# Kernel tuning notes

Measured on AMD Instinct MI355X. Metric: run time of the kernel, lower is better.

## Reference

```python
import jax, jax.numpy as jnp
import numpy as np

B, T, C = 4, 128, 512
NH, HS = 8, 64          # n_head, head_dim = C // NH
ORDER = 3               # attention_order
SCALE = 1.0 / np.sqrt(HS)


def setup_inputs() -> dict:
    key = jax.random.key(0)
    ks = jax.random.split(key, 7)
    s = 0.02
    return {
        "x": jax.random.normal(ks[0], (B, T, C), jnp.float32),
        "Wp0": jax.random.normal(ks[1], (C, C), jnp.float32) * s,
        "Wp1": jax.random.normal(ks[2], (C, C), jnp.float32) * s,
        "Wp2": jax.random.normal(ks[3], (C, C), jnp.float32) * s,
        "Wv0": jax.random.normal(ks[4], (HS, HS), jnp.float32) * s,
        "Wv1": jax.random.normal(ks[5], (HS, HS), jnp.float32) * s,
        "Wc": jax.random.normal(ks[6], (C, C), jnp.float32) * s,
    }


def _heads(x, W):
    # Linear then split heads: (B,T,C) -> (B,NH,T,HS)
    return (x @ W).reshape(B, T, NH, HS).transpose(0, 2, 1, 3)


def _causal_mask(t, order):
    # indices grid [T]^order, True where i0 >= i1 >= ... >= i_{order-1}
    idx = jnp.arange(t)
    g = jnp.stack(jnp.meshgrid(*([idx] * order), indexing='ij'), axis=-1)
    return jnp.all(jnp.diff(g, axis=-1) <= 0, axis=-1)


def reference(x, Wp0, Wp1, Wp2, Wv0, Wv1, Wc):
    p0 = _heads(x, Wp0)  # (B,NH,T,HS)
    p1 = _heads(x, Wp1)
    p2 = _heads(x, Wp2)

    # pairwise scores, then higher-order broadcast exactly as the torch einsum
    # ('bh...i,bhkd->bh...ik' sums the key over d and broadcasts — faithful).
    att = jnp.einsum('bhid,bhjd->bhij', p0, p1) * SCALE        # (B,NH,T,T)
    att = jnp.einsum('bh...i,bhkd->bh...ik', att, p2)          # (B,NH,T,T,T)

    mask = _causal_mask(T, ORDER)[None, None]                  # (1,1,T,T,T)
    att = jnp.where(mask, att, -jnp.inf)
    att = jax.nn.softmax(att.reshape(B, NH, T, T * T), axis=-1)

    # value tensors with broadcasted elementwise product over the order dims
    V0 = (p1 @ Wv0)[:, :, :, None, :]   # (B,NH,T,1,HS)
    V1 = (p2 @ Wv1)[:, :, None, :, :]   # (B,NH,1,T,HS)
    V = (V0 * V1).reshape(B, NH, T * T, HS)

    y = jnp.einsum('bhij,bhjd->bhid', att, V)                  # (B,NH,T,HS)
    y = y.transpose(0, 2, 1, 3).reshape(B, T, C)
    return y @ Wc
```

## Files before the change

kernel.cpp:

```cpp
#include <hip/hip_runtime.h>
#include <hip/hip_bf16.h>
#include <math.h>

#define B 4
#define T 128
#define C 512
#define NH 8
#define HS 64
#define BH (B*NH)

typedef __attribute__((ext_vector_type(8))) short bf16x8;
typedef __attribute__((ext_vector_type(4))) float f32x4;

__device__ __forceinline__ unsigned short bfc(float x) {
    return __builtin_bit_cast(unsigned short, __float2bfloat16(x));
}
__device__ __forceinline__ unsigned int pk_bf16(float a, float b) {
    return (unsigned int)bfc(a) | ((unsigned int)bfc(b) << 16);
}
__device__ __forceinline__ float lo_f(unsigned int g) {
    return __builtin_bit_cast(float, g << 16);
}
__device__ __forceinline__ float hi_f(unsigned int g) {
    return __builtin_bit_cast(float, g & 0xffff0000u);
}

__global__ __launch_bounds__(256) void proj_kernel(
    const float* __restrict__ X,
    const float* __restrict__ Wp0, const float* __restrict__ Wp1, const float* __restrict__ Wp2,
    unsigned short* __restrict__ p0b, unsigned short* __restrict__ p1b,
    unsigned short* __restrict__ p2b, float* __restrict__ rr)
{
    __shared__ __align__(16) unsigned short As[64][72];
    __shared__ __align__(16) unsigned short Bs[64][72];
    __shared__ float Ls[64][69];
    __shared__ float sRS[4][64];
    const int z = blockIdx.z;
    const float* W = (z == 0) ? Wp0 : (z == 1) ? Wp1 : Wp2;
    const int m0 = blockIdx.y * 64, n0 = blockIdx.x * 64;
    const int tid = threadIdx.x;
    const int w = tid >> 6, lane = tid & 63, quad = lane >> 4, l16 = lane & 15;
    f32x4 acc[4];
    #pragma unroll
    for (int mt = 0; mt < 4; ++mt) acc[mt] = (f32x4){0.f, 0.f, 0.f, 0.f};

    for (int k0 = 0; k0 < 512; k0 += 64) {
        __syncthreads();
        #pragma unroll
        for (int it = 0; it < 2; ++it) {
            const int q = tid + it * 256;
            const int row = q >> 3, c8 = (q & 7) * 8;
            const float4 a = *(const float4*)&X[(size_t)(m0 + row) * 512 + k0 + c8];
            const float4 b = *(const float4*)&X[(size_t)(m0 + row) * 512 + k0 + c8 + 4];
            uint4 o;
            o.x = pk_bf16(a.x, a.y);
            o.y = pk_bf16(a.z, a.w);
            o.z = pk_bf16(b.x, b.y);
            o.w = pk_bf16(b.z, b.w);
            *(uint4*)&As[row][c8] = o;
        }
        #pragma unroll
        for (int it = 0; it < 4; ++it) {
            const int q = tid + it * 256;
            const int row = q >> 4, c4 = (q & 15) * 4;
            const float4 v = *(const float4*)&W[(size_t)(k0 + row) * 512 + n0 + c4];
            Ls[row][c4 + 0] = v.x; Ls[row][c4 + 1] = v.y;
            Ls[row][c4 + 2] = v.z; Ls[row][c4 + 3] = v.w;
        }
        __syncthreads();
        #pragma unroll
        for (int it = 0; it < 2; ++it) {
            const int q = tid + it * 256;
            const int nrow = q >> 3, k8 = (q & 7) * 8;
            uint4 o;
            o.x = pk_bf16(Ls[k8 + 0][nrow], Ls[k8 + 1][nrow]);
            o.y = pk_bf16(Ls[k8 + 2][nrow], Ls[k8 + 3][nrow]);
            o.z = pk_bf16(Ls[k8 + 4][nrow], Ls[k8 + 5][nrow]);
            o.w = pk_bf16(Ls[k8 + 6][nrow], Ls[k8 + 7][nrow]);
            *(uint4*)&Bs[nrow][k8] = o;
        }
        __syncthreads();
        #pragma unroll
        for (int kt = 0; kt < 2; ++kt) {
            const bf16x8 b8 = *(const bf16x8*)&Bs[w * 16 + l16][kt * 32 + quad * 8];
            #pragma unroll
            for (int mt = 0; mt < 4; ++mt) {
                const bf16x8 a8 = *(const bf16x8*)&As[mt * 16 + l16][kt * 32 + quad * 8];
                acc[mt] = __builtin_amdgcn_mfma_f32_16x16x32_bf16(a8, b8, acc[mt], 0, 0, 0);
            }
        }
    }

    {
        const int n = n0 + w * 16 + l16;
        const int h = n >> 6, d = n & 63;
        unsigned short* pz = (z == 0) ? p0b : (z == 1) ? p1b : p2b;
        #pragma unroll
        for (int mt = 0; mt < 4; ++mt) {
            #pragma unroll
            for (int r = 0; r < 4; ++r) {
                const int m = m0 + mt * 16 + quad * 4 + r;
                const int bb = m >> 7, t = m & 127;
                pz[((size_t)(bb * NH + h) * T + t) * HS + d] = bfc(acc[mt][r]);
            }
        }
    }
    if (z == 2) {
        #pragma unroll
        for (int mt = 0; mt < 4; ++mt)
            #pragma unroll
            for (int r = 0; r < 4; ++r) {
                float v = acc[mt][r];
                v += __shfl_xor(v, 1, 64); v += __shfl_xor(v, 2, 64);
                v += __shfl_xor(v, 4, 64); v += __shfl_xor(v, 8, 64);
                if (l16 == 0) sRS[w][mt * 16 + quad * 4 + r] = v;
            }
        __syncthreads();
        if (tid < 64) {
            const float s = sRS[0][tid] + sRS[1][tid] + sRS[2][tid] + sRS[3][tid];
            const int m = m0 + tid, bb = m >> 7, tl = m & 127, h = n0 >> 6;
            rr[(bb * NH + h) * T + tl] = s;
        }
    }
}

__global__ __launch_bounds__(256) void attn_kernel(
    const unsigned short* __restrict__ p0b, const unsigned short* __restrict__ p1b,
    const unsigned short* __restrict__ p2b, const float* __restrict__ rr,
    const float* __restrict__ Wv0, const float* __restrict__ Wv1,
    unsigned short* __restrict__ Yb)
{
    __shared__ __align__(16) unsigned short sV0T[64][136];
    __shared__ __align__(16) unsigned short sV1T[64][136];
    __shared__ __align__(16) union {
        unsigned short sWvT[2][64][72];
        struct { unsigned short sE[128 * 64]; float sS[8][128]; } e;
    } u;
    __shared__ float srr[128];
    __shared__ float sZ[4];

    const int bid = blockIdx.x;
    const int bh = bid & (BH - 1);
    const int ig = bid >> 5;
    const int tid = threadIdx.x;
    const int w = tid >> 6;
    const int lane = tid & 63;
    const int quad = lane >> 4;
    const int l16 = lane & 15;

    if (tid < 128) srr[tid] = rr[bh * T + tid];

    #pragma unroll
    for (int v = 0; v < 2; ++v) {
        const float* Wv = v ? Wv1 : Wv0;
        #pragma unroll
        for (int it = 0; it < 4; ++it) {
            const int k = (tid >> 4) + it * 16;
            const int d0 = (tid & 15) * 4;
            const float4 wv = *(const float4*)&Wv[(size_t)k * 64 + d0];
            u.sWvT[v][d0 + 0][k] = bfc(wv.x);
            u.sWvT[v][d0 + 1][k] = bfc(wv.y);
            u.sWvT[v][d0 + 2][k] = bfc(wv.z);
            u.sWvT[v][d0 + 3][k] = bfc(wv.w);
        }
    }
    __syncthreads();

    #pragma unroll
    for (int v = 0; v < 2; ++v) {
        const unsigned short* pg = v ? p2b : p1b;
        unsigned short (*dst)[136] = v ? sV1T : sV0T;
        #pragma unroll
        for (int nn = 0; nn < 2; ++nn) {
            const int nt = w + nn * 4;
            f32x4 vacc[4];
            #pragma unroll
            for (int mt = 0; mt < 4; ++mt) vacc[mt] = (f32x4){0.f, 0.f, 0.f, 0.f};
            #pragma unroll
            for (int kt = 0; kt < 2; ++kt) {
                const bf16x8 b8 = *(const bf16x8*)&pg[((size_t)bh * T + nt * 16 + l16) * HS + kt * 32 + quad * 8];
                #pragma unroll
                for (int mt = 0; mt < 4; ++mt) {
                    const bf16x8 a8 = *(const bf16x8*)&u.sWvT[v][mt * 16 + l16][kt * 32 + quad * 8];
                    vacc[mt] = __builtin_amdgcn_mfma_f32_16x16x32_bf16(a8, b8, vacc[mt], 0, 0, 0);
                }
            }
            #pragma unroll
            for (int mt = 0; mt < 4; ++mt)
                #pragma unroll
                for (int r = 0; r < 4; ++r)
                    dst[mt * 16 + quad * 4 + r][nt * 16 + l16] = bfc(vacc[mt][r]);
        }
    }
    __syncthreads();

    uint4 v1r[4];
    #pragma unroll
    for (int kt = 0; kt < 4; ++kt)
        v1r[kt] = *(const uint4*)&sV1T[(w << 4) + l16][(quad << 3) + (kt << 5)];

    {
        const int qr = l16 & 7;
        const int irow = (qr & 1) ? (16 * qr + 15 - ig) : (16 * qr + ig);
        const unsigned short* ap = p0b + ((size_t)bh * T + irow) * HS + (quad << 3);
        const unsigned short* bp = p1b + (size_t)bh * T * HS + (quad << 3);
        f32x4 s0 = (f32x4){0.f, 0.f, 0.f, 0.f};
        f32x4 s1 = (f32x4){0.f, 0.f, 0.f, 0.f};
        #pragma unroll
        for (int kt = 0; kt < 2; ++kt) {
            const bf16x8 a8 = *(const bf16x8*)(ap + (kt << 5));
            const bf16x8 b0 = *(const bf16x8*)(bp + (size_t)((w << 5) + l16) * HS + (kt << 5));
            const bf16x8 b1 = *(const bf16x8*)(bp + (size_t)((w << 5) + 16 + l16) * HS + (kt << 5));
            s0 = __builtin_amdgcn_mfma_f32_16x16x32_bf16(a8, b0, s0, 0, 0, 0);
            s1 = __builtin_amdgcn_mfma_f32_16x16x32_bf16(a8, b1, s1, 0, 0, 0);
        }
        if (quad < 2) {
            #pragma unroll
            for (int r = 0; r < 4; ++r) {
                u.e.sS[quad * 4 + r][(w << 5) + l16]      = s0[r] * 0.125f;
                u.e.sS[quad * 4 + r][(w << 5) + 16 + l16] = s1[r] * 0.125f;
            }
        }
    }
    __syncthreads();

    const float L2E = 1.4426950408889634f;

    for (int qq = 7; qq >= 0; --qq) {
        const int i = (qq & 1) ? (16 * qq + 15 - ig) : (16 * qq + ig);
        const float* sSq = u.e.sS[qq];

        float mhat;
        {
            float a0 = (lane <= i) ? fabsf(sSq[lane]) : 0.f;
            float a1 = (64 + lane <= i) ? fabsf(sSq[64 + lane]) : 0.f;
            float r0 = (lane <= i) ? fabsf(srr[lane]) : 0.f;
            float r1 = (64 + lane <= i) ? fabsf(srr[64 + lane]) : 0.f;
            float aS = fmaxf(a0, a1), aR = fmaxf(r0, r1);
            #pragma unroll
            for (int off = 32; off; off >>= 1) {
                aS = fmaxf(aS, __shfl_xor(aS, off, 64));
                aR = fmaxf(aR, __shfl_xor(aR, off, 64));
            }
            mhat = aS * aR;
        }

        const float bexp = -mhat * L2E;
        const int mtmax = i >> 4;
        const int cc = tid & 7;
        const int rowin = tid >> 3;
        const int k0l = cc << 3;
        float zacc = 0.f;

        float rk[8];
        *(float4*)&rk[0] = *(const float4*)&srr[k0l];
        *(float4*)&rk[4] = *(const float4*)&srr[k0l + 4];
        const int npass0 = (mtmax >> 1) + 1;
        for (int p = 0; p < npass0; ++p) {
            const int jj = (p << 5) + rowin;
            uint4 o = {0u, 0u, 0u, 0u};
            if (jj <= i && k0l <= jj) {
                const float aL = sSq[jj] * L2E;
                const int dlim = jj - k0l;
                float e[8];
                #pragma unroll
                for (int q = 0; q < 8; ++q) {
                    const float ex = __builtin_amdgcn_exp2f(fmaf(aL, rk[q], bexp));
                    e[q] = (q <= dlim) ? ex : 0.f;
                    zacc += e[q];
                }
                o.x = pk_bf16(e[0], e[1]);
                o.y = pk_bf16(e[2], e[3]);
                o.z = pk_bf16(e[4], e[5]);
                o.w = pk_bf16(e[6], e[7]);
            }
            *(uint4*)&u.e.sE[(jj << 6) + ((cc ^ (jj & 7)) << 3)] = o;
        }

        f32x4 acc[8];
        #pragma unroll
        for (int mt = 0; mt < 8; ++mt) acc[mt] = (f32x4){0.f, 0.f, 0.f, 0.f};

        if (mtmax < 4) {
            #pragma unroll
            for (int off = 32; off; off >>= 1) zacc += __shfl_xor(zacc, off, 64);
            if (lane == 0) sZ[w] = zacc;
            __syncthreads();
            #pragma unroll
            for (int mt = 0; mt < 4; ++mt) {
                if (mt <= mtmax) {
                    #pragma unroll
                    for (int kt = 0; kt <= 1; ++kt) {
                        if (kt <= (mt >> 1)) {
                            const int swz = ((kt << 2) + quad) ^ (l16 & 7);
                            const bf16x8 a8 = *(const bf16x8*)&u.e.sE[(((mt << 4) + l16) << 6) + (swz << 3)];
                            acc[mt] = __builtin_amdgcn_mfma_f32_16x16x32_bf16(
                                a8, __builtin_bit_cast(bf16x8, v1r[kt]), acc[mt], 0, 0, 0);
                        }
                    }
                }
            }
        } else {
            __syncthreads();
            #pragma unroll
            for (int mt = 0; mt < 8; ++mt) {
                if (mt <= mtmax) {
                    #pragma unroll
                    for (int kt = 0; kt <= 1; ++kt) {
                        if (kt <= (mt >> 1)) {
                            const int swz = ((kt << 2) + quad) ^ (l16 & 7);
                            const bf16x8 a8 = *(const bf16x8*)&u.e.sE[(((mt << 4) + l16) << 6) + (swz << 3)];
                            acc[mt] = __builtin_amdgcn_mfma_f32_16x16x32_bf16(
                                a8, __builtin_bit_cast(bf16x8, v1r[kt]), acc[mt], 0, 0, 0);
                        }
                    }
                }
            }
            __syncthreads();
            *(float4*)&rk[0] = *(const float4*)&srr[64 + k0l];
            *(float4*)&rk[4] = *(const float4*)&srr[64 + k0l + 4];
            const int npass1 = ((mtmax - 4) >> 1) + 1;
            for (int p = 0; p < npass1; ++p) {
                const int jj = 64 + (p << 5) + rowin;
                uint4 o = {0u, 0u, 0u, 0u};
                if (jj <= i && 64 + k0l <= jj) {
                    const float aL = sSq[jj] * L2E;
                    const int dlim = jj - 64 - k0l;
                    float e[8];
                    #pragma unroll
                    for (int q = 0; q < 8; ++q) {
                        const float ex = __builtin_amdgcn_exp2f(fmaf(aL, rk[q], bexp));
                        e[q] = (q <= dlim) ? ex : 0.f;
                        zacc += e[q];
                    }
                    o.x = pk_bf16(e[0], e[1]);
                    o.y = pk_bf16(e[2], e[3]);
                    o.z = pk_bf16(e[4], e[5]);
                    o.w = pk_bf16(e[6], e[7]);
                }
                *(uint4*)&u.e.sE[(jj << 6) + ((cc ^ (jj & 7)) << 3)] = o;
            }
            #pragma unroll
            for (int off = 32; off; off >>= 1) zacc += __shfl_xor(zacc, off, 64);
            if (lane == 0) sZ[w] = zacc;
            __syncthreads();
            #pragma unroll
            for (int mt = 4; mt < 8; ++mt) {
                if (mt <= mtmax) {
                    #pragma unroll
                    for (int kt = 2; kt <= 3; ++kt) {
                        if (kt <= (mt >> 1)) {
                            const int swz = (((kt & 1) << 2) + quad) ^ (l16 & 7);
                            const bf16x8 a8 = *(const bf16x8*)&u.e.sE[(((mt << 4) + l16) << 6) + (swz << 3)];
                            acc[mt] = __builtin_amdgcn_mfma_f32_16x16x32_bf16(
                                a8, __builtin_bit_cast(bf16x8, v1r[kt]), acc[mt], 0, 0, 0);
                        }
                    }
                }
            }
        }
        const float Z = sZ[0] + sZ[1] + sZ[2] + sZ[3];

        const unsigned short* v0row = sV0T[(w << 4) + l16];
        float part = 0.f;
        #pragma unroll
        for (int mt = 0; mt < 8; ++mt) {
            if (mt < mtmax) {
                const uint2 uu = *(const uint2*)&v0row[(mt << 4) + (quad << 2)];
                part = fmaf(lo_f(uu.x), acc[mt][0], part);
                part = fmaf(hi_f(uu.x), acc[mt][1], part);
                part = fmaf(lo_f(uu.y), acc[mt][2], part);
                part = fmaf(hi_f(uu.y), acc[mt][3], part);
            } else if (mt == mtmax) {
                const uint2 uu = *(const uint2*)&v0row[(mt << 4) + (quad << 2)];
                const int jb = (mt << 4) + (quad << 2);
                if (jb + 0 <= i) part = fmaf(lo_f(uu.x), acc[mt][0], part);
                if (jb + 1 <= i) part = fmaf(hi_f(uu.x), acc[mt][1], part);
                if (jb + 2 <= i) part = fmaf(lo_f(uu.y), acc[mt][2], part);
                if (jb + 3 <= i) part = fmaf(hi_f(uu.y), acc[mt][3], part);
            }
        }
        part += __shfl_xor(part, 16, 64);
        part += __shfl_xor(part, 32, 64);
        if (lane < 16) {
            const int bb = bh >> 3, hh = bh & 7;
            Yb[((size_t)(bb * T + i) * C) + hh * HS + (w << 4) + l16] = bfc(part / Z);
        }
        __syncthreads();
    }
}

__global__ __launch_bounds__(256) void outmm_kernel(
    const unsigned short* __restrict__ Ab, const float* __restrict__ Wc,
    float* __restrict__ OUT)
{
    __shared__ __align__(16) unsigned short As[64][72];
    __shared__ __align__(16) unsigned short Bs[64][72];
    __shared__ float Ls[64][69];
    const int m0 = blockIdx.y * 64, n0 = blockIdx.x * 64;
    const int tid = threadIdx.x;
    const int w = tid >> 6, lane = tid & 63, quad = lane >> 4, l16 = lane & 15;
    f32x4 acc[4];
    #pragma unroll
    for (int mt = 0; mt < 4; ++mt) acc[mt] = (f32x4){0.f, 0.f, 0.f, 0.f};
    for (int k0 = 0; k0 < 512; k0 += 64) {
        __syncthreads();
        #pragma unroll
        for (int it = 0; it < 2; ++it) {
            const int q = tid + it * 256;
            const int row = q >> 3, c8 = (q & 7) * 8;
            *(uint4*)&As[row][c8] = *(const uint4*)&Ab[(size_t)(m0 + row) * 512 + k0 + c8];
        }
        #pragma unroll
        for (int it = 0; it < 4; ++it) {
            const int q = tid + it * 256;
            const int row = q >> 4, c4 = (q & 15) * 4;
            const float4 v = *(const float4*)&Wc[(size_t)(k0 + row) * 512 + n0 + c4];
            Ls[row][c4 + 0] = v.x; Ls[row][c4 + 1] = v.y;
            Ls[row][c4 + 2] = v.z; Ls[row][c4 + 3] = v.w;
        }
        __syncthreads();
        #pragma unroll
        for (int it = 0; it < 2; ++it) {
            const int q = tid + it * 256;
            const int nrow = q >> 3, k8 = (q & 7) * 8;
            uint4 o;
            o.x = pk_bf16(Ls[k8 + 0][nrow], Ls[k8 + 1][nrow]);
            o.y = pk_bf16(Ls[k8 + 2][nrow], Ls[k8 + 3][nrow]);
            o.z = pk_bf16(Ls[k8 + 4][nrow], Ls[k8 + 5][nrow]);
            o.w = pk_bf16(Ls[k8 + 6][nrow], Ls[k8 + 7][nrow]);
            *(uint4*)&Bs[nrow][k8] = o;
        }
        __syncthreads();
        #pragma unroll
        for (int kt = 0; kt < 2; ++kt) {
            const bf16x8 b8 = *(const bf16x8*)&Bs[w * 16 + l16][kt * 32 + quad * 8];
            #pragma unroll
            for (int mt = 0; mt < 4; ++mt) {
                const bf16x8 a8 = *(const bf16x8*)&As[mt * 16 + l16][kt * 32 + quad * 8];
                acc[mt] = __builtin_amdgcn_mfma_f32_16x16x32_bf16(a8, b8, acc[mt], 0, 0, 0);
            }
        }
    }
    const int n = n0 + w * 16 + l16;
    #pragma unroll
    for (int mt = 0; mt < 4; ++mt)
        #pragma unroll
        for (int r = 0; r < 4; ++r) {
            const int mrow = m0 + mt * 16 + quad * 4 + r;
            OUT[(size_t)mrow * 512 + n] = acc[mt][r];
        }
}

extern "C" void kernel_launch(void* const* d_in, const int* in_sizes, int n_in,
                              void* d_out, int out_size, void* d_ws, size_t ws_size,
                              hipStream_t stream)
{
    const float* x   = (const float*)d_in[0];
    const float* Wp0 = (const float*)d_in[1];
    const float* Wp1 = (const float*)d_in[2];
    const float* Wp2 = (const float*)d_in[3];
    const float* Wv0 = (const float*)d_in[4];
    const float* Wv1 = (const float*)d_in[5];
    const float* Wc  = (const float*)d_in[6];
    float* out = (float*)d_out;

    char* w8 = (char*)d_ws;
    const size_t HB = 512 * 1024;
    unsigned short* p0b = (unsigned short*)(w8 + 0 * HB);
    unsigned short* p1b = (unsigned short*)(w8 + 1 * HB);
    unsigned short* p2b = (unsigned short*)(w8 + 2 * HB);
    unsigned short* Yb  = (unsigned short*)(w8 + 3 * HB);
    float*          rr  = (float*)        (w8 + 4 * HB);

    proj_kernel <<<dim3(8, 8, 3), 256, 0, stream>>>(x, Wp0, Wp1, Wp2, p0b, p1b, p2b, rr);
    attn_kernel <<<dim3(512), 256, 0, stream>>>(p0b, p1b, p2b, rr, Wv0, Wv1, Yb);
    outmm_kernel<<<dim3(8, 8), 256, 0, stream>>>(Yb, Wc, out);
}
```

Baseline: 116.4 us.

## Fuse output projection into attention kernel via per-head atomic accumulation

```diff
diff --git a/kernel.cpp b/kernel.cpp
--- a/kernel.cpp
+++ b/kernel.cpp
@@ -29,7 +29,7 @@
     const float* __restrict__ X,
     const float* __restrict__ Wp0, const float* __restrict__ Wp1, const float* __restrict__ Wp2,
     unsigned short* __restrict__ p0b, unsigned short* __restrict__ p1b,
-    unsigned short* __restrict__ p2b, float* __restrict__ rr)
+    unsigned short* __restrict__ p2b, float* __restrict__ rr, float* __restrict__ OUT)
 {
     __shared__ __align__(16) unsigned short As[64][72];
     __shared__ __align__(16) unsigned short Bs[64][72];
@@ -40,6 +40,16 @@
     const int m0 = blockIdx.y * 64, n0 = blockIdx.x * 64;
     const int tid = threadIdx.x;
     const int w = tid >> 6, lane = tid & 63, quad = lane >> 4, l16 = lane & 15;
+
+    {
+        const int fid = z * 64 + (int)blockIdx.y * 8 + (int)blockIdx.x;
+        if (fid < 128) {
+            float4 zz = {0.f, 0.f, 0.f, 0.f};
+            *(float4*)&OUT[(size_t)fid * 2048 + tid * 8]     = zz;
+            *(float4*)&OUT[(size_t)fid * 2048 + tid * 8 + 4] = zz;
+        }
+    }
+
     f32x4 acc[4];
     #pragma unroll
     for (int mt = 0; mt < 4; ++mt) acc[mt] = (f32x4){0.f, 0.f, 0.f, 0.f};
@@ -128,7 +138,7 @@
     const unsigned short* __restrict__ p0b, const unsigned short* __restrict__ p1b,
     const unsigned short* __restrict__ p2b, const float* __restrict__ rr,
     const float* __restrict__ Wv0, const float* __restrict__ Wv1,
-    unsigned short* __restrict__ Yb)
+    const float* __restrict__ Wc, float* __restrict__ OUT)
 {
     __shared__ __align__(16) unsigned short sV0T[64][136];
     __shared__ __align__(16) unsigned short sV1T[64][136];
@@ -138,6 +148,7 @@
     } u;
     __shared__ float srr[128];
     __shared__ float sZ[4];
+    __shared__ float sY[8][64];
 
     const int bid = blockIdx.x;
     const int bh = bid & (BH - 1);
@@ -382,74 +393,34 @@
         }
         part += __shfl_xor(part, 16, 64);
         part += __shfl_xor(part, 32, 64);
-        if (lane < 16) {
-            const int bb = bh >> 3, hh = bh & 7;
-            Yb[((size_t)(bb * T + i) * C) + hh * HS + (w << 4) + l16] = bfc(part / Z);
-        }
+        if (lane < 16) sY[qq][(w << 4) + l16] = part / Z;
         __syncthreads();
     }
-}
-
-__global__ __launch_bounds__(256) void outmm_kernel(
-    const unsigned short* __restrict__ Ab, const float* __restrict__ Wc,
-    float* __restrict__ OUT)
-{
-    __shared__ __align__(16) unsigned short As[64][72];
-    __shared__ __align__(16) unsigned short Bs[64][72];
-    __shared__ float Ls[64][69];
-    const int m0 = blockIdx.y * 64, n0 = blockIdx.x * 64;
-    const int tid = threadIdx.x;
-    const int w = tid >> 6, lane = tid & 63, quad = lane >> 4, l16 = lane & 15;
-    f32x4 acc[4];
-    #pragma unroll
-    for (int mt = 0; mt < 4; ++mt) acc[mt] = (f32x4){0.f, 0.f, 0.f, 0.f};
-    for (int k0 = 0; k0 < 512; k0 += 64) {
-        __syncthreads();
-        #pragma unroll
-        for (int it = 0; it < 2; ++it) {
-            const int q = tid + it * 256;
-            const int row = q >> 3, c8 = (q & 7) * 8;
-            *(uint4*)&As[row][c8] = *(const uint4*)&Ab[(size_t)(m0 + row) * 512 + k0 + c8];
-        }
-        #pragma unroll
-        for (int it = 0; it < 4; ++it) {
-            const int q = tid + it * 256;
-            const int row = q >> 4, c4 = (q & 15) * 4;
-            const float4 v = *(const float4*)&Wc[(size_t)(k0 + row) * 512 + n0 + c4];
-            Ls[row][c4 + 0] = v.x; Ls[row][c4 + 1] = v.y;
-            Ls[row][c4 + 2] = v.z; Ls[row][c4 + 3] = v.w;
-        }
-        __syncthreads();
-        #pragma unroll
-        for (int it = 0; it < 2; ++it) {
-            const int q = tid + it * 256;
-            const int nrow = q >> 3, k8 = (q & 7) * 8;
-            uint4 o;
-            o.x = pk_bf16(Ls[k8 + 0][nrow], Ls[k8 + 1][nrow]);
-            o.y = pk_bf16(Ls[k8 + 2][nrow], Ls[k8 + 3][nrow]);
-            o.z = pk_bf16(Ls[k8 + 4][nrow], Ls[k8 + 5][nrow]);
-            o.w = pk_bf16(Ls[k8 + 6][nrow], Ls[k8 + 7][nrow]);
-            *(uint4*)&Bs[nrow][k8] = o;
-        }
-        __syncthreads();
-        #pragma unroll
-        for (int kt = 0; kt < 2; ++kt) {
-            const bf16x8 b8 = *(const bf16x8*)&Bs[w * 16 + l16][kt * 32 + quad * 8];
-            #pragma unroll
-            for (int mt = 0; mt < 4; ++mt) {
-                const bf16x8 a8 = *(const bf16x8*)&As[mt * 16 + l16][kt * 32 + quad * 8];
-                acc[mt] = __builtin_amdgcn_mfma_f32_16x16x32_bf16(a8, b8, acc[mt], 0, 0, 0);
-            }
-        }
-    }
-    const int n = n0 + w * 16 + l16;
-    #pragma unroll
-    for (int mt = 0; mt < 4; ++mt)
-        #pragma unroll
-        for (int r = 0; r < 4; ++r) {
-            const int mrow = m0 + mt * 16 + quad * 4 + r;
-            OUT[(size_t)mrow * 512 + n] = acc[mt][r];
-        }
+
+    {
+        const int bb = bh >> 3, hh = bh & 7;
+        const int n0 = tid * 2;
+        float oacc[8][2];
+        #pragma unroll
+        for (int r = 0; r < 8; ++r) { oacc[r][0] = 0.f; oacc[r][1] = 0.f; }
+        const float* wc = Wc + (size_t)hh * 64 * 512 + n0;
+        for (int k = 0; k < 64; ++k) {
+            const float2 wv = *(const float2*)&wc[(size_t)k * 512];
+            #pragma unroll
+            for (int r = 0; r < 8; ++r) {
+                const float yv = sY[r][k];
+                oacc[r][0] = fmaf(yv, wv.x, oacc[r][0]);
+                oacc[r][1] = fmaf(yv, wv.y, oacc[r][1]);
+            }
+        }
+        #pragma unroll
+        for (int qq = 0; qq < 8; ++qq) {
+            const int i = (qq & 1) ? (16 * qq + 15 - ig) : (16 * qq + ig);
+            float* orow = OUT + (size_t)(bb * T + i) * 512 + n0;
+            atomicAdd(&orow[0], oacc[qq][0]);
+            atomicAdd(&orow[1], oacc[qq][1]);
+        }
+    }
 }
 
 extern "C" void kernel_launch(void* const* d_in, const int* in_sizes, int n_in,
@@ -470,10 +441,8 @@
     unsigned short* p0b = (unsigned short*)(w8 + 0 * HB);
     unsigned short* p1b = (unsigned short*)(w8 + 1 * HB);
     unsigned short* p2b = (unsigned short*)(w8 + 2 * HB);
-    unsigned short* Yb  = (unsigned short*)(w8 + 3 * HB);
-    float*          rr  = (float*)        (w8 + 4 * HB);
-
-    proj_kernel <<<dim3(8, 8, 3), 256, 0, stream>>>(x, Wp0, Wp1, Wp2, p0b, p1b, p2b, rr);
-    attn_kernel <<<dim3(512), 256, 0, stream>>>(p0b, p1b, p2b, rr, Wv0, Wv1, Yb);
-    outmm_kernel<<<dim3(8, 8), 256, 0, stream>>>(Yb, Wc, out);
-}
+    float*          rr  = (float*)        (w8 + 3 * HB);
+
+    proj_kernel <<<dim3(8, 8, 3), 256, 0, stream>>>(x, Wp0, Wp1, Wp2, p0b, p1b, p2b, rr, out);
+    attn_kernel <<<dim3(512), 256, 0, stream>>>(p0b, p1b, p2b, rr, Wv0, Wv1, Wc, out);
+}
```

After: 120.1 us. 1.03x slower.

## Double attention grid, halve rows per block, single-pass full-width exp tile

Applied to the files above, without the earlier changes.

```diff
diff --git a/kernel.cpp b/kernel.cpp
--- a/kernel.cpp
+++ b/kernel.cpp
@@ -130,12 +130,14 @@
     const float* __restrict__ Wv0, const float* __restrict__ Wv1,
     unsigned short* __restrict__ Yb)
 {
-    __shared__ __align__(16) unsigned short sV0T[64][136];
-    __shared__ __align__(16) unsigned short sV1T[64][136];
     __shared__ __align__(16) union {
-        unsigned short sWvT[2][64][72];
-        struct { unsigned short sE[128 * 64]; float sS[8][128]; } e;
+        struct {
+            unsigned short sWv[64][72];
+            unsigned short sVst[64][136];
+        } v;
+        unsigned short sE[128 * 128];
     } u;
+    __shared__ float sS[4][128];
     __shared__ float srr[128];
     __shared__ float sZ[4];
 
@@ -151,57 +153,83 @@
     if (tid < 128) srr[tid] = rr[bh * T + tid];
 
     #pragma unroll
-    for (int v = 0; v < 2; ++v) {
-        const float* Wv = v ? Wv1 : Wv0;
-        #pragma unroll
-        for (int it = 0; it < 4; ++it) {
-            const int k = (tid >> 4) + it * 16;
-            const int d0 = (tid & 15) * 4;
-            const float4 wv = *(const float4*)&Wv[(size_t)k * 64 + d0];
-            u.sWvT[v][d0 + 0][k] = bfc(wv.x);
-            u.sWvT[v][d0 + 1][k] = bfc(wv.y);
-            u.sWvT[v][d0 + 2][k] = bfc(wv.z);
-            u.sWvT[v][d0 + 3][k] = bfc(wv.w);
-        }
+    for (int it = 0; it < 4; ++it) {
+        const int k = (tid >> 4) + it * 16;
+        const int d0 = (tid & 15) * 4;
+        const float4 wv = *(const float4*)&Wv0[(size_t)k * 64 + d0];
+        u.v.sWv[d0 + 0][k] = bfc(wv.x); u.v.sWv[d0 + 1][k] = bfc(wv.y);
+        u.v.sWv[d0 + 2][k] = bfc(wv.z); u.v.sWv[d0 + 3][k] = bfc(wv.w);
     }
     __syncthreads();
 
     #pragma unroll
-    for (int v = 0; v < 2; ++v) {
-        const unsigned short* pg = v ? p2b : p1b;
-        unsigned short (*dst)[136] = v ? sV1T : sV0T;
-        #pragma unroll
-        for (int nn = 0; nn < 2; ++nn) {
-            const int nt = w + nn * 4;
-            f32x4 vacc[4];
-            #pragma unroll
-            for (int mt = 0; mt < 4; ++mt) vacc[mt] = (f32x4){0.f, 0.f, 0.f, 0.f};
-            #pragma unroll
-            for (int kt = 0; kt < 2; ++kt) {
-                const bf16x8 b8 = *(const bf16x8*)&pg[((size_t)bh * T + nt * 16 + l16) * HS + kt * 32 + quad * 8];
-                #pragma unroll
-                for (int mt = 0; mt < 4; ++mt) {
-                    const bf16x8 a8 = *(const bf16x8*)&u.sWvT[v][mt * 16 + l16][kt * 32 + quad * 8];
-                    vacc[mt] = __builtin_amdgcn_mfma_f32_16x16x32_bf16(a8, b8, vacc[mt], 0, 0, 0);
-                }
-            }
-            #pragma unroll
-            for (int mt = 0; mt < 4; ++mt)
-                #pragma unroll
-                for (int r = 0; r < 4; ++r)
-                    dst[mt * 16 + quad * 4 + r][nt * 16 + l16] = bfc(vacc[mt][r]);
-        }
+    for (int nn = 0; nn < 2; ++nn) {
+        const int nt = w + nn * 4;
+        f32x4 vacc[4];
+        #pragma unroll
+        for (int mt = 0; mt < 4; ++mt) vacc[mt] = (f32x4){0.f, 0.f, 0.f, 0.f};
+        #pragma unroll
+        for (int kt = 0; kt < 2; ++kt) {
+            const bf16x8 b8 = *(const bf16x8*)&p1b[((size_t)bh * T + nt * 16 + l16) * HS + kt * 32 + quad * 8];
+            #pragma unroll
+            for (int mt = 0; mt < 4; ++mt) {
+                const bf16x8 a8 = *(const bf16x8*)&u.v.sWv[mt * 16 + l16][kt * 32 + quad * 8];
+                vacc[mt] = __builtin_amdgcn_mfma_f32_16x16x32_bf16(a8, b8, vacc[mt], 0, 0, 0);
+            }
+        }
+        #pragma unroll
+        for (int mt = 0; mt < 4; ++mt)
+            #pragma unroll
+            for (int r = 0; r < 4; ++r)
+                u.v.sVst[mt * 16 + quad * 4 + r][nt * 16 + l16] = bfc(vacc[mt][r]);
     }
     __syncthreads();
 
+    uint2 v0r[8];
+    #pragma unroll
+    for (int mt = 0; mt < 8; ++mt)
+        v0r[mt] = *(const uint2*)&u.v.sVst[(w << 4) + l16][(mt << 4) + (quad << 2)];
+    #pragma unroll
+    for (int it = 0; it < 4; ++it) {
+        const int k = (tid >> 4) + it * 16;
+        const int d0 = (tid & 15) * 4;
+        const float4 wv = *(const float4*)&Wv1[(size_t)k * 64 + d0];
+        u.v.sWv[d0 + 0][k] = bfc(wv.x); u.v.sWv[d0 + 1][k] = bfc(wv.y);
+        u.v.sWv[d0 + 2][k] = bfc(wv.z); u.v.sWv[d0 + 3][k] = bfc(wv.w);
+    }
+    __syncthreads();
+
+    #pragma unroll
+    for (int nn = 0; nn < 2; ++nn) {
+        const int nt = w + nn * 4;
+        f32x4 vacc[4];
+        #pragma unroll
+        for (int mt = 0; mt < 4; ++mt) vacc[mt] = (f32x4){0.f, 0.f, 0.f, 0.f};
+        #pragma unroll
+        for (int kt = 0; kt < 2; ++kt) {
+            const bf16x8 b8 = *(const bf16x8*)&p2b[((size_t)bh * T + nt * 16 + l16) * HS + kt * 32 + quad * 8];
+            #pragma unroll
+            for (int mt = 0; mt < 4; ++mt) {
+                const bf16x8 a8 = *(const bf16x8*)&u.v.sWv[mt * 16 + l16][kt * 32 + quad * 8];
+                vacc[mt] = __builtin_amdgcn_mfma_f32_16x16x32_bf16(a8, b8, vacc[mt], 0, 0, 0);
+            }
+        }
+        #pragma unroll
+        for (int mt = 0; mt < 4; ++mt)
+            #pragma unroll
+            for (int r = 0; r < 4; ++r)
+                u.v.sVst[mt * 16 + quad * 4 + r][nt * 16 + l16] = bfc(vacc[mt][r]);
+    }
+    __syncthreads();
+
     uint4 v1r[4];
     #pragma unroll
     for (int kt = 0; kt < 4; ++kt)
-        v1r[kt] = *(const uint4*)&sV1T[(w << 4) + l16][(quad << 3) + (kt << 5)];
+        v1r[kt] = *(const uint4*)&u.v.sVst[(w << 4) + l16][(quad << 3) + (kt << 5)];
 
     {
-        const int qr = l16 & 7;
-        const int irow = (qr & 1) ? (16 * qr + 15 - ig) : (16 * qr + ig);
+        const int qr = l16 & 3;
+        const int irow = (qr & 1) ? (32 * qr + 31 - ig) : (32 * qr + ig);
         const unsigned short* ap = p0b + ((size_t)bh * T + irow) * HS + (quad << 3);
         const unsigned short* bp = p1b + (size_t)bh * T * HS + (quad << 3);
         f32x4 s0 = (f32x4){0.f, 0.f, 0.f, 0.f};
@@ -214,11 +242,11 @@
             s0 = __builtin_amdgcn_mfma_f32_16x16x32_bf16(a8, b0, s0, 0, 0, 0);
             s1 = __builtin_amdgcn_mfma_f32_16x16x32_bf16(a8, b1, s1, 0, 0, 0);
         }
-        if (quad < 2) {
+        if (quad == 0) {
             #pragma unroll
             for (int r = 0; r < 4; ++r) {
-                u.e.sS[quad * 4 + r][(w << 5) + l16]      = s0[r] * 0.125f;
-                u.e.sS[quad * 4 + r][(w << 5) + 16 + l16] = s1[r] * 0.125f;
+                sS[r][(w << 5) + l16]      = s0[r] * 0.125f;
+                sS[r][(w << 5) + 16 + l16] = s1[r] * 0.125f;
             }
         }
     }
@@ -226,9 +254,9 @@
 
     const float L2E = 1.4426950408889634f;
 
-    for (int qq = 7; qq >= 0; --qq) {
-        const int i = (qq & 1) ? (16 * qq + 15 - ig) : (16 * qq + ig);
-        const float* sSq = u.e.sS[qq];
+    for (int qq = 3; qq >= 0; --qq) {
+        const int i = (qq & 1) ? (32 * qq + 31 - ig) : (32 * qq + ig);
+        const float* sSq = sS[qq];
 
         float mhat;
         {
@@ -247,17 +275,17 @@
 
         const float bexp = -mhat * L2E;
         const int mtmax = i >> 4;
-        const int cc = tid & 7;
-        const int rowin = tid >> 3;
+        const int cc = tid & 15;
+        const int rowin = tid >> 4;
         const int k0l = cc << 3;
         float zacc = 0.f;
 
         float rk[8];
         *(float4*)&rk[0] = *(const float4*)&srr[k0l];
         *(float4*)&rk[4] = *(const float4*)&srr[k0l + 4];
-        const int npass0 = (mtmax >> 1) + 1;
-        for (int p = 0; p < npass0; ++p) {
-            const int jj = (p << 5) + rowin;
+        const int npass = mtmax + 1;
+        for (int p = 0; p < npass; ++p) {
+            const int jj = (p << 4) + rowin;
             uint4 o = {0u, 0u, 0u, 0u};
             if (jj <= i && k0l <= jj) {
                 const float aL = sSq[jj] * L2E;
@@ -274,105 +302,43 @@
                 o.z = pk_bf16(e[4], e[5]);
                 o.w = pk_bf16(e[6], e[7]);
             }
-            *(uint4*)&u.e.sE[(jj << 6) + ((cc ^ (jj & 7)) << 3)] = o;
-        }
+            *(uint4*)&u.sE[(jj << 7) + ((cc ^ (jj & 7)) << 3)] = o;
+        }
+        #pragma unroll
+        for (int off = 32; off; off >>= 1) zacc += __shfl_xor(zacc, off, 64);
+        if (lane == 0) sZ[w] = zacc;
+        __syncthreads();
 
         f32x4 acc[8];
         #pragma unroll
         for (int mt = 0; mt < 8; ++mt) acc[mt] = (f32x4){0.f, 0.f, 0.f, 0.f};
-
-        if (mtmax < 4) {
-            #pragma unroll
-            for (int off = 32; off; off >>= 1) zacc += __shfl_xor(zacc, off, 64);
-            if (lane == 0) sZ[w] = zacc;
-            __syncthreads();
-            #pragma unroll
-            for (int mt = 0; mt < 4; ++mt) {
-                if (mt <= mtmax) {
-                    #pragma unroll
-                    for (int kt = 0; kt <= 1; ++kt) {
-                        if (kt <= (mt >> 1)) {
-                            const int swz = ((kt << 2) + quad) ^ (l16 & 7);
-                            const bf16x8 a8 = *(const bf16x8*)&u.e.sE[(((mt << 4) + l16) << 6) + (swz << 3)];
-                            acc[mt] = __builtin_amdgcn_mfma_f32_16x16x32_bf16(
-                                a8, __builtin_bit_cast(bf16x8, v1r[kt]), acc[mt], 0, 0, 0);
-                        }
+        #pragma unroll
+        for (int mt = 0; mt < 8; ++mt) {
+            if (mt <= mtmax) {
+                #pragma unroll
+                for (int kt = 0; kt < 4; ++kt) {
+                    if (kt <= (mt >> 1)) {
+                        const int ch = ((kt << 2) + quad) ^ (l16 & 7);
+                        const bf16x8 a8 = *(const bf16x8*)&u.sE[(((mt << 4) + l16) << 7) + (ch << 3)];
+                        acc[mt] = __builtin_amdgcn_mfma_f32_16x16x32_bf16(
+                            a8, __builtin_bit_cast(bf16x8, v1r[kt]), acc[mt], 0, 0, 0);
                     }
                 }
             }
-        } else {
-            __syncthreads();
-            #pragma unroll
-            for (int mt = 0; mt < 8; ++mt) {
-                if (mt <= mtmax) {
-                    #pragma unroll
-                    for (int kt = 0; kt <= 1; ++kt) {
-                        if (kt <= (mt >> 1)) {
-                            const int swz = ((kt << 2) + quad) ^ (l16 & 7);
-                            const bf16x8 a8 = *(const bf16x8*)&u.e.sE[(((mt << 4) + l16) << 6) + (swz << 3)];
-                            acc[mt] = __builtin_amdgcn_mfma_f32_16x16x32_bf16(
-                                a8, __builtin_bit_cast(bf16x8, v1r[kt]), acc[mt], 0, 0, 0);
-                        }
-                    }
-                }
-            }
-            __syncthreads();
-            *(float4*)&rk[0] = *(const float4*)&srr[64 + k0l];
-            *(float4*)&rk[4] = *(const float4*)&srr[64 + k0l + 4];
-            const int npass1 = ((mtmax - 4) >> 1) + 1;
-            for (int p = 0; p < npass1; ++p) {
-                const int jj = 64 + (p << 5) + rowin;
-                uint4 o = {0u, 0u, 0u, 0u};
-                if (jj <= i && 64 + k0l <= jj) {
-                    const float aL = sSq[jj] * L2E;
-                    const int dlim = jj - 64 - k0l;
-                    float e[8];
-                    #pragma unroll
-                    for (int q = 0; q < 8; ++q) {
-                        const float ex = __builtin_amdgcn_exp2f(fmaf(aL, rk[q], bexp));
-                        e[q] = (q <= dlim) ? ex : 0.f;
-                        zacc += e[q];
-                    }
-                    o.x = pk_bf16(e[0], e[1]);
-                    o.y = pk_bf16(e[2], e[3]);
-                    o.z = pk_bf16(e[4], e[5]);
-                    o.w = pk_bf16(e[6], e[7]);
-                }
-                *(uint4*)&u.e.sE[(jj << 6) + ((cc ^ (jj & 7)) << 3)] = o;
-            }
-            #pragma unroll
-            for (int off = 32; off; off >>= 1) zacc += __shfl_xor(zacc, off, 64);
-            if (lane == 0) sZ[w] = zacc;
-            __syncthreads();
-            #pragma unroll
-            for (int mt = 4; mt < 8; ++mt) {
-                if (mt <= mtmax) {
-                    #pragma unroll
-                    for (int kt = 2; kt <= 3; ++kt) {
-                        if (kt <= (mt >> 1)) {
-                            const int swz = (((kt & 1) << 2) + quad) ^ (l16 & 7);
-                            const bf16x8 a8 = *(const bf16x8*)&u.e.sE[(((mt << 4) + l16) << 6) + (swz << 3)];
-                            acc[mt] = __builtin_amdgcn_mfma_f32_16x16x32_bf16(
-                                a8, __builtin_bit_cast(bf16x8, v1r[kt]), acc[mt], 0, 0, 0);
-                        }
-                    }
-                }
-            }
         }
         const float Z = sZ[0] + sZ[1] + sZ[2] + sZ[3];
 
-        const unsigned short* v0row = sV0T[(w << 4) + l16];
         float part = 0.f;
         #pragma unroll
         for (int mt = 0; mt < 8; ++mt) {
             if (mt < mtmax) {
-                const uint2 uu = *(const uint2*)&v0row[(mt << 4) + (quad << 2)];
+                const uint2 uu = v0r[mt];
                 part = fmaf(lo_f(uu.x), acc[mt][0], part);
                 part = fmaf(hi_f(uu.x), acc[mt][1], part);
                 part = fmaf(lo_f(uu.y), acc[mt][2], part);
                 part = fmaf(hi_f(uu.y), acc[mt][3], part);
             } else if (mt == mtmax) {
-                const uint2 uu = *(const uint2*)&v0row[(mt << 4) + (quad << 2)];
+                const uint2 uu = v0r[mt];
                 const int jb = (mt << 4) + (quad << 2);
                 if (jb + 0 <= i) part = fmaf(lo_f(uu.x), acc[mt][0], part);
                 if (jb + 1 <= i) part = fmaf(hi_f(uu.x), acc[mt][1], part);
@@ -474,6 +440,6 @@
     float*          rr  = (float*)        (w8 + 4 * HB);
 
     proj_kernel <<<dim3(8, 8, 3), 256, 0, stream>>>(x, Wp0, Wp1, Wp2, p0b, p1b, p2b, rr);
-    attn_kernel <<<dim3(512), 256, 0, stream>>>(p0b, p1b, p2b, rr, Wv0, Wv1, Yb);
+    attn_kernel <<<dim3(1024), 256, 0, stream>>>(p0b, p1b, p2b, rr, Wv0, Wv1, Yb);
     outmm_kernel<<<dim3(8, 8), 256, 0, stream>>>(Yb, Wc, out);
 }
```

New measurement: 125.4 us. 7.7% more time.
